# Kernel optimization log

Measured on AMD Instinct MI355X. Metric: run time of the kernel, lower is better.

## Reference

```python
import jax, jax.numpy as jnp
import numpy as np

NUM_CLASSES = 19
M = 5
TEMP = 100.0
MIN_RATIO = 0.75
IGNORE = 255
LOG2PI = float(np.log(2.0 * np.pi))


def l2_normalize(x, eps=1e-12):
    n = jnp.linalg.norm(x, axis=-1, keepdims=True)
    return x / jnp.maximum(n, eps)


def downscale_label_ratio(gt, scale):
    # gt: [B, H, W] int labels with IGNORE; avg-pool one-hot, keep majority class
    B, H, W = gt.shape
    out = jnp.where(gt == IGNORE, NUM_CLASSES, gt)
    oh = jax.nn.one_hot(out, NUM_CLASSES + 1, dtype=jnp.float32)  # [B,H,W,C+1]
    h, w = H // scale, W // scale
    pooled = oh.reshape(B, h, scale, w, scale, NUM_CLASSES + 1).mean(axis=(2, 4))
    ratio = pooled.max(axis=-1)          # [B,h,w] majority-class ratio
    idx = jnp.argmax(pooled, axis=-1)    # first max, like torch.max
    idx = jnp.where(idx == NUM_CLASSES, IGNORE, idx)
    idx = jnp.where(ratio < MIN_RATIO, IGNORE, idx)
    return idx


def gmm_log_prob(x, loc, scale):
    # Diagonal-Gaussian log-prob of x:[N,A] under K components loc/scale:[K,A] -> [N,K]
    inv_var = 1.0 / (scale * scale)
    maha = ((x * x) @ inv_var.T
            - 2.0 * (x @ (loc * inv_var).T)
            + jnp.sum(loc * loc * inv_var, axis=-1)[None, :])
    log_det = 2.0 * jnp.sum(jnp.log(scale), axis=-1)  # [K]
    A = x.shape[-1]
    return -0.5 * (A * LOG2PI + log_det[None, :] + maha)


def setup_inputs() -> dict:
    key = jax.random.key(0)
    ks = jax.random.split(key, 8)
    B, A, Hf, Wf = 4, 64, 256, 256
    Hm = Wm = 1024
    feat = jax.random.normal(ks[0], (B, A, Hf, Wf), jnp.float32)
    lab = jax.random.randint(ks[1], (B, Hm, Wm), 0, NUM_CLASSES)
    ign = jax.random.uniform(ks[2], (B, Hm, Wm)) < 0.05
    mask = jnp.where(ign, IGNORE, lab).astype(jnp.int32)
    mean = jax.random.normal(ks[3], (NUM_CLASSES, M, A), jnp.float32)
    covariance = 0.5 + jax.random.uniform(ks[4], (NUM_CLASSES, M, A), jnp.float32)
    target_memory = jax.random.normal(ks[5], (NUM_CLASSES, A, 100), jnp.float32)
    class_target = jax.random.uniform(ks[6], (NUM_CLASSES,), jnp.float32)
    class_sourse = 0.1 + jax.random.uniform(ks[7], (NUM_CLASSES,), jnp.float32)
    return {"feat": feat, "mask": mask, "mean": mean, "covariance": covariance,
            "target_memory": target_memory, "class_target": class_target,
            "class_sourse": class_sourse}


def reference(feat, mask, mean, covariance, target_memory, class_target, class_sourse):
    # ProtoGMM_loss: source=False, target_memory is not None, weak_target=False
    B, A, Hf, Wf = feat.shape
    scale = mask.shape[-1] // Wf
    m = downscale_label_ratio(mask, scale).reshape(-1)          # [N]
    f = feat.transpose(0, 2, 3, 1).reshape(-1, A)               # [N,A]
    f = l2_normalize(f)
    fd = jax.lax.stop_gradient(f)                               # feat.detach()
    loc = jax.lax.stop_gradient(mean).reshape(-1, A)            # [C*M,A]
    sc = jax.lax.stop_gradient(covariance).reshape(-1, A)

    log_prob = gmm_log_prob(fd, loc, sc)                        # [N,C*M]
    value = jax.nn.softmax(log_prob, axis=-1).reshape(-1, NUM_CLASSES, M)
    dist_ratio = jnp.nan_to_num(jax.lax.stop_gradient(class_target)
                                / jax.lax.stop_gradient(class_sourse))
    value = dist_ratio[None, :, None] * value                   # class-ratio scaling
    mean_target = l2_normalize(jax.lax.stop_gradient(target_memory).mean(axis=2))  # [C,A]
    sim = jax.nn.softmax(fd @ mean_target.T, axis=-1)           # [N,C]
    value = value * sim[:, :, None]
    labels = jnp.argmax(value.sum(-1), axis=-1)                 # pseudo-labels [N]

    logits = (f @ loc.T / TEMP).reshape(-1, NUM_CLASSES, M)     # [N,C,M]
    logits_max = logits.max(-1)                                 # [N,C]
    logls = jax.nn.log_softmax(logits_max, axis=-1)
    ce = -jnp.take_along_axis(logls, labels[:, None], axis=1)[:, 0]  # [N]
    valid = (m != IGNORE)
    loss = jnp.sum(jnp.where(valid, ce, 0.0)) / jnp.maximum(
        jnp.sum(valid).astype(jnp.float32), 1.0)
    return loss
```

## Files before the change

### kernel.cpp

```cpp
#include <hip/hip_runtime.h>
#include <hip/hip_bf16.h>
#include <math.h>

#define NCLS 19
#define MCOMP 5
#define AFEAT 64
#define IGNORE_L 255
#define LOG2PI 1.8378770664093453f

#define ROWS 160
#define WAM_B 0
#define WAL_B 40960
#define CST_B 61440
#define MT_B  62080
#define DR_B  64640
#define ACC_B 64768
#define VAL_B 64832

typedef __attribute__((ext_vector_type(8))) short bf16x8;
typedef __attribute__((ext_vector_type(4))) float f32x4;

__device__ inline float b2f(short s) {
    return __uint_as_float(((unsigned int)(unsigned short)s) << 16);
}
__device__ inline short f2b(float f) {
    __hip_bfloat16 h = __float2bfloat16(f);
    return *reinterpret_cast<short*>(&h);
}

__global__ void precompute_kernel(const float* __restrict__ mean,
                                  const float* __restrict__ cov,
                                  const float* __restrict__ tmem,
                                  const float* __restrict__ ct,
                                  const float* __restrict__ cs,
                                  char* __restrict__ wsb) {
    int blk = blockIdx.x;
    int a = threadIdx.x;
    short* wam = (short*)(wsb + WAM_B);
    short* wal = (short*)(wsb + WAL_B);
    float* cst = (float*)(wsb + CST_B);
    short* mtb = (short*)(wsb + MT_B);
    float* dr  = (float*)(wsb + DR_B);
    float* acc = (float*)(wsb + ACC_B);

    if (blk < ROWS) {
        int r = blk, c = r >> 3, m = r & 7;
        if (c < NCLS && m < MCOMP) {
            int k = c * MCOMP + m;
            float lo = mean[k * AFEAT + a];
            float cv = cov[k * AFEAT + a];
            float iv = 1.0f / (cv * cv);
            wam[r * 128 + a]      = f2b(-2.0f * lo * iv);
            wam[r * 128 + 64 + a] = f2b(iv);
            wal[r * 64 + a]       = f2b(lo);
            float s1 = lo * lo * iv;
            float s2 = logf(cv);
            for (int off = 32; off > 0; off >>= 1) {
                s1 += __shfl_xor(s1, off, 64);
                s2 += __shfl_xor(s2, off, 64);
            }
            if (a == 0) cst[r] = AFEAT * LOG2PI + 2.0f * s2 + s1;
        } else {
            wam[r * 128 + a] = 0; wam[r * 128 + 64 + a] = 0;
            wal[r * 64 + a] = 0;
            if (a == 0) cst[r] = 1e30f;
        }
    } else if (blk < ROWS + 20) {
        int c = blk - ROWS;
        if (c < NCLS) {
            const float* p = tmem + ((size_t)c * AFEAT + a) * 100;
            float s = 0.f;
            for (int j = 0; j < 100; ++j) s += p[j];
            s *= 0.01f;
            float n2 = s * s;
            for (int off = 32; off > 0; off >>= 1) n2 += __shfl_xor(n2, off, 64);
            float den = fmaxf(sqrtf(n2), 1e-12f);
            mtb[c * AFEAT + a] = f2b(s / den);
        } else {
            mtb[c * AFEAT + a] = 0;
        }
    } else {
        if (a < 20) {
            float r = 0.f;
            if (a < NCLS) {
                r = ct[a] / cs[a];
                if (isnan(r)) r = 0.f;
                else if (isinf(r)) r = (r > 0.f) ? 3.402823466e38f : -3.402823466e38f;
            }
            dr[a] = r;
        }
        if (a == 32) { acc[0] = 0.f; acc[1] = 0.f; }
    }
}

__global__ void valid_kernel(const int* __restrict__ mask,
                             unsigned long long* __restrict__ vwords) {
    int n = blockIdx.x * 256 + threadIdx.x;
    int b = n >> 16, rem = n & 65535, y = rem >> 8, x = rem & 255;
    const int* mp = mask + (((size_t)b << 10) + ((size_t)y << 2)) * 1024 + ((size_t)x << 2);
    int v[16];
#pragma unroll
    for (int r = 0; r < 4; ++r) {
        int4 q = *reinterpret_cast<const int4*>(mp + (size_t)r * 1024);
        v[r * 4 + 0] = q.x; v[r * 4 + 1] = q.y; v[r * 4 + 2] = q.z; v[r * 4 + 3] = q.w;
    }
    bool valid = false;
#pragma unroll
    for (int i = 0; i < 16; ++i) {
        int cnt = 0;
#pragma unroll
        for (int j = 0; j < 16; ++j) cnt += (v[j] == v[i]) ? 1 : 0;
        if (v[i] != IGNORE_L && cnt >= 12) valid = true;
    }
    unsigned long long bm = __ballot(valid);
    if ((threadIdx.x & 63) == 0) vwords[n >> 6] = bm;
}

__global__ __launch_bounds__(512, 2)
void protogmm_kernel(const float* __restrict__ feat,
                     const char* __restrict__ wsb,
                     const unsigned long long* __restrict__ vwords,
                     float* __restrict__ accg) {
    __shared__ short wamL[ROWS * 128];
    __shared__ short walL[ROWS * 64];
    __shared__ float cstL[ROWS];
    __shared__ short mtL[20 * 64];
    __shared__ float drL[20];

    int tid = threadIdx.x;
    {
        const uint4* s0 = (const uint4*)(wsb + WAM_B);
        for (int i = tid; i < 2560; i += 512) {
            int row = i >> 4, slot = i & 15;
            *(uint4*)((char*)wamL + row * 256 + ((slot ^ (row & 7)) << 4)) = s0[i];
        }
        const uint4* s1 = (const uint4*)(wsb + WAL_B);
        for (int i = tid; i < 1280; i += 512) {
            int row = i >> 3, slot = i & 7;
            *(uint4*)((char*)walL + row * 128 + ((slot ^ (row & 7)) << 4)) = s1[i];
        }
        const float* s2 = (const float*)(wsb + CST_B);
        for (int i = tid; i < ROWS; i += 512) cstL[i] = s2[i];
        const uint4* s3 = (const uint4*)(wsb + MT_B);
        for (int i = tid; i < 160; i += 512) ((uint4*)mtL)[i] = s3[i];
        const float* s4 = (const float*)(wsb + DR_B);
        if (tid < 20) drL[tid] = s4[tid];
    }
    __syncthreads();

    int lane = tid & 63, l15 = lane & 15, g = lane >> 4, rx = l15 & 7;
    int wv = blockIdx.x * 8 + (tid >> 6);
    int p = g >> 1;

    float cesum = 0.f, cntsum = 0.f;

#pragma unroll 1
    for (int it = 0; it < 4; ++it) {
        int tile = wv * 4 + it;
        int n0 = tile << 4;
        int b = n0 >> 16, y = (n0 >> 8) & 255, x0 = n0 & 255;

        bf16x8 F[4];
        {
            const float* fb = feat + (size_t)b * (AFEAT * 65536) + y * 256 + x0 + l15;
            float fa[8], fc[8];
            float n2 = 0.f;
#pragma unroll
            for (int j = 0; j < 8; ++j) {
                fa[j] = fb[(size_t)(8 * g + j) * 65536];
                fc[j] = fb[(size_t)(32 + 8 * g + j) * 65536];
            }
#pragma unroll
            for (int j = 0; j < 8; ++j) {
                n2 = fmaf(fa[j], fa[j], n2);
                n2 = fmaf(fc[j], fc[j], n2);
            }
            n2 += __shfl_xor(n2, 16, 64);
            n2 += __shfl_xor(n2, 32, 64);
            float inv = 1.0f / fmaxf(sqrtf(n2), 1e-12f);
#pragma unroll
            for (int j = 0; j < 8; ++j) {
                float u = fa[j] * inv, w2 = fc[j] * inv;
                F[0][j] = f2b(u);
                F[1][j] = f2b(w2);
                F[2][j] = f2b(u * u);
                F[3][j] = f2b(w2 * w2);
            }
        }

        float grun = -1e30f;
        float bestv = -1.0f, bestc = 0.f, bestl = 0.f, ls = 0.f;

#pragma unroll 1
        for (int t = 0; t < 10; ++t) {
            f32x4 acc = *(const f32x4*)(cstL + 16 * t + 4 * g);
#pragma unroll
            for (int kt = 0; kt < 4; ++kt) {
                bf16x8 wa = *(const bf16x8*)((char*)wamL + (16 * t + l15) * 256 +
                                             (((4 * kt + g) ^ rx) << 4));
                acc = __builtin_amdgcn_mfma_f32_16x16x32_bf16(wa, F[kt], acc, 0, 0, 0);
            }

            f32x4 a2 = {0.f, 0.f, 0.f, 0.f};
#pragma unroll
            for (int kt = 0; kt < 2; ++kt) {
                bf16x8 wl = *(const bf16x8*)((char*)walL + (16 * t + l15) * 128 +
                                             (((4 * kt + g) ^ rx) << 4));
                a2 = __builtin_amdgcn_mfma_f32_16x16x32_bf16(wl, F[kt], a2, 0, 0, 0);
            }
            float d0 = a2[0] * 0.01f, d1 = a2[1] * 0.01f;
            float d2 = a2[2] * 0.01f, d3 = a2[3] * 0.01f;
            if (g & 1) { d1 = -1e30f; d2 = -1e30f; d3 = -1e30f; }
            float lt = fmaxf(fmaxf(d0, d1), fmaxf(d2, d3));
            if (t == 9 && (g & 2)) lt = -1e30f;
            float lmx = fmaxf(lt, __shfl_xor(lt, 16, 64));
            ls += __expf(lmx);

            float mn = fminf(fminf(acc[0], acc[1]), fminf(acc[2], acc[3]));
            mn = fminf(mn, __shfl_xor(mn, 16, 64));
            mn = fminf(mn, __shfl_xor(mn, 32, 64));
            float gnew = fmaxf(grun, -0.5f * mn);
            float sold = __expf(grun - gnew);

            float e0 = __expf(fmaf(acc[0], -0.5f, -gnew));
            float e1 = __expf(fmaf(acc[1], -0.5f, -gnew));
            float e2 = __expf(fmaf(acc[2], -0.5f, -gnew));
            float e3 = __expf(fmaf(acc[3], -0.5f, -gnew));
            float st = (e0 + e1) + (e2 + e3);
            float Sc = st + __shfl_xor(st, 16, 64);

            const short* m0a = mtL + (2 * t) * 64 + 8 * g;
            const short* m1a = mtL + (2 * t + 1) * 64 + 8 * g;
            float p0 = 0.f, p1 = 0.f;
#pragma unroll
            for (int j = 0; j < 8; ++j) {
                float u = b2f(F[0][j]), w2 = b2f(F[1][j]);
                p0 = fmaf(u, b2f(m0a[j]), p0);
                p0 = fmaf(w2, b2f(m0a[32 + j]), p0);
                p1 = fmaf(u, b2f(m1a[j]), p1);
                p1 = fmaf(w2, b2f(m1a[32 + j]), p1);
            }
            p0 += __shfl_xor(p0, 16, 64); p0 += __shfl_xor(p0, 32, 64);
            p1 += __shfl_xor(p1, 16, 64); p1 += __shfl_xor(p1, 32, 64);
            float sd = p ? p1 : p0;

            float val = drL[2 * t + p] * __expf(sd) * Sc;
            bestv *= sold;
            if (val > bestv) { bestv = val; bestc = (float)(2 * t + p); bestl = lmx; }
            grun = gnew;
        }

        {
            float ov = __shfl_xor(bestv, 32, 64);
            float oc = __shfl_xor(bestc, 32, 64);
            float ol = __shfl_xor(bestl, 32, 64);
            bool take = (ov > bestv) || (ov == bestv && oc < bestc);
            bestv = take ? ov : bestv;
            bestl = take ? ol : bestl;
            bestc = take ? oc : bestc;
            ls += __shfl_xor(ls, 32, 64);
        }
        float ce = __logf(ls) - bestl;

        unsigned long long w = vwords[tile >> 2];
        float vb = (float)((w >> ((n0 & 63) + l15)) & 1ull);
        float own = (g == 0) ? 1.f : 0.f;
        cesum  = fmaf(own * vb, ce, cesum);
        cntsum += own * vb;
    }

#pragma unroll
    for (int off = 32; off > 0; off >>= 1) {
        cesum  += __shfl_xor(cesum, off, 64);
        cntsum += __shfl_xor(cntsum, off, 64);
    }
    if (lane == 0) {
        atomicAdd(&accg[0], cesum);
        atomicAdd(&accg[1], cntsum);
    }
}

__global__ void finalize_kernel(const float* __restrict__ acc, float* __restrict__ out) {
    out[0] = acc[0] / fmaxf(acc[1], 1.0f);
}

extern "C" void kernel_launch(void* const* d_in, const int* in_sizes, int n_in,
                              void* d_out, int out_size, void* d_ws, size_t ws_size,
                              hipStream_t stream) {
    const float* feat = (const float*)d_in[0];
    const int*   mask = (const int*)d_in[1];
    const float* mean = (const float*)d_in[2];
    const float* cov  = (const float*)d_in[3];
    const float* tmem = (const float*)d_in[4];
    const float* ct   = (const float*)d_in[5];
    const float* cs   = (const float*)d_in[6];
    float* out = (float*)d_out;
    char*  wsb = (char*)d_ws;

    precompute_kernel<<<ROWS + 20 + 1, 64, 0, stream>>>(mean, cov, tmem, ct, cs, wsb);
    valid_kernel<<<1024, 256, 0, stream>>>(mask, (unsigned long long*)(wsb + VAL_B));
    protogmm_kernel<<<512, 512, 0, stream>>>(feat, wsb,
                                             (const unsigned long long*)(wsb + VAL_B),
                                             (float*)(wsb + ACC_B));
    finalize_kernel<<<1, 1, 0, stream>>>((const float*)(wsb + ACC_B), out);
}
```

Before: 248.9 us.

## Process two pixel tiles per iteration and score classes in log domain

```diff
diff --git a/kernel.cpp b/kernel.cpp
--- a/kernel.cpp
+++ b/kernel.cpp
@@ -116,7 +116,7 @@
     if ((threadIdx.x & 63) == 0) vwords[n >> 6] = bm;
 }
 
-__global__ __launch_bounds__(512, 2)
+__global__ __launch_bounds__(512, 4)
 void protogmm_kernel(const float* __restrict__ feat,
                      const char* __restrict__ wsb,
                      const unsigned long long* __restrict__ vwords,
@@ -125,7 +125,7 @@
     __shared__ short walL[ROWS * 64];
     __shared__ float cstL[ROWS];
     __shared__ short mtL[20 * 64];
-    __shared__ float drL[20];
+    __shared__ float ldrL[20];
 
     int tid = threadIdx.x;
     {
@@ -144,7 +144,7 @@
         const uint4* s3 = (const uint4*)(wsb + MT_B);
         for (int i = tid; i < 160; i += 512) ((uint4*)mtL)[i] = s3[i];
         const float* s4 = (const float*)(wsb + DR_B);
-        if (tid < 20) drL[tid] = s4[tid];
+        if (tid < 20) ldrL[tid] = __logf(s4[tid]);
     }
     __syncthreads();
 
@@ -155,118 +155,164 @@
     float cesum = 0.f, cntsum = 0.f;
 
 #pragma unroll 1
-    for (int it = 0; it < 4; ++it) {
-        int tile = wv * 4 + it;
-        int n0 = tile << 4;
+    for (int it = 0; it < 2; ++it) {
+        int n0 = (wv * 2 + it) << 5;
         int b = n0 >> 16, y = (n0 >> 8) & 255, x0 = n0 & 255;
 
-        bf16x8 F[4];
+        bf16x8 FA[4], FB[4];
         {
             const float* fb = feat + (size_t)b * (AFEAT * 65536) + y * 256 + x0 + l15;
-            float fa[8], fc[8];
-            float n2 = 0.f;
+            float aa[8], ac[8], ba[8], bc[8];
+            float nA = 0.f, nB = 0.f;
 #pragma unroll
             for (int j = 0; j < 8; ++j) {
-                fa[j] = fb[(size_t)(8 * g + j) * 65536];
-                fc[j] = fb[(size_t)(32 + 8 * g + j) * 65536];
+                aa[j] = fb[(size_t)(8 * g + j) * 65536];
+                ac[j] = fb[(size_t)(32 + 8 * g + j) * 65536];
+                ba[j] = fb[(size_t)(8 * g + j) * 65536 + 16];
+                bc[j] = fb[(size_t)(32 + 8 * g + j) * 65536 + 16];
             }
 #pragma unroll
             for (int j = 0; j < 8; ++j) {
-                n2 = fmaf(fa[j], fa[j], n2);
-                n2 = fmaf(fc[j], fc[j], n2);
-            }
-            n2 += __shfl_xor(n2, 16, 64);
-            n2 += __shfl_xor(n2, 32, 64);
-            float inv = 1.0f / fmaxf(sqrtf(n2), 1e-12f);
+                nA = fmaf(aa[j], aa[j], nA); nA = fmaf(ac[j], ac[j], nA);
+                nB = fmaf(ba[j], ba[j], nB); nB = fmaf(bc[j], bc[j], nB);
+            }
+            nA += __shfl_xor(nA, 16, 64); nA += __shfl_xor(nA, 32, 64);
+            nB += __shfl_xor(nB, 16, 64); nB += __shfl_xor(nB, 32, 64);
+            float iA = 1.0f / fmaxf(sqrtf(nA), 1e-12f);
+            float iB = 1.0f / fmaxf(sqrtf(nB), 1e-12f);
 #pragma unroll
             for (int j = 0; j < 8; ++j) {
-                float u = fa[j] * inv, w2 = fc[j] * inv;
-                F[0][j] = f2b(u);
-                F[1][j] = f2b(w2);
-                F[2][j] = f2b(u * u);
-                F[3][j] = f2b(w2 * w2);
-            }
-        }
-
-        float grun = -1e30f;
-        float bestv = -1.0f, bestc = 0.f, bestl = 0.f, ls = 0.f;
-
-#pragma unroll 1
+                float u, w2;
+                u = aa[j] * iA; w2 = ac[j] * iA;
+                FA[0][j] = f2b(u); FA[1][j] = f2b(w2);
+                FA[2][j] = f2b(u * u); FA[3][j] = f2b(w2 * w2);
+                u = ba[j] * iB; w2 = bc[j] * iB;
+                FB[0][j] = f2b(u); FB[1][j] = f2b(w2);
+                FB[2][j] = f2b(u * u); FB[3][j] = f2b(w2 * w2);
+            }
+        }
+
+        float bWA = -3.4e38f, bcA = 0.f, blA = 0.f, lsA = 0.f;
+        float bWB = -3.4e38f, bcB = 0.f, blB = 0.f, lsB = 0.f;
+
+#pragma unroll 2
         for (int t = 0; t < 10; ++t) {
-            f32x4 acc = *(const f32x4*)(cstL + 16 * t + 4 * g);
+            f32x4 cini = *(const f32x4*)(cstL + 16 * t + 4 * g);
+            f32x4 aA = cini, aB = cini;
 #pragma unroll
             for (int kt = 0; kt < 4; ++kt) {
                 bf16x8 wa = *(const bf16x8*)((char*)wamL + (16 * t + l15) * 256 +
                                              (((4 * kt + g) ^ rx) << 4));
-                acc = __builtin_amdgcn_mfma_f32_16x16x32_bf16(wa, F[kt], acc, 0, 0, 0);
-            }
-
-            f32x4 a2 = {0.f, 0.f, 0.f, 0.f};
+                aA = __builtin_amdgcn_mfma_f32_16x16x32_bf16(wa, FA[kt], aA, 0, 0, 0);
+                aB = __builtin_amdgcn_mfma_f32_16x16x32_bf16(wa, FB[kt], aB, 0, 0, 0);
+            }
+            f32x4 qA = {0.f, 0.f, 0.f, 0.f}, qB = {0.f, 0.f, 0.f, 0.f};
 #pragma unroll
             for (int kt = 0; kt < 2; ++kt) {
                 bf16x8 wl = *(const bf16x8*)((char*)walL + (16 * t + l15) * 128 +
                                              (((4 * kt + g) ^ rx) << 4));
-                a2 = __builtin_amdgcn_mfma_f32_16x16x32_bf16(wl, F[kt], a2, 0, 0, 0);
-            }
-            float d0 = a2[0] * 0.01f, d1 = a2[1] * 0.01f;
-            float d2 = a2[2] * 0.01f, d3 = a2[3] * 0.01f;
-            if (g & 1) { d1 = -1e30f; d2 = -1e30f; d3 = -1e30f; }
-            float lt = fmaxf(fmaxf(d0, d1), fmaxf(d2, d3));
-            if (t == 9 && (g & 2)) lt = -1e30f;
-            float lmx = fmaxf(lt, __shfl_xor(lt, 16, 64));
-            ls += __expf(lmx);
-
-            float mn = fminf(fminf(acc[0], acc[1]), fminf(acc[2], acc[3]));
-            mn = fminf(mn, __shfl_xor(mn, 16, 64));
-            mn = fminf(mn, __shfl_xor(mn, 32, 64));
-            float gnew = fmaxf(grun, -0.5f * mn);
-            float sold = __expf(grun - gnew);
-
-            float e0 = __expf(fmaf(acc[0], -0.5f, -gnew));
-            float e1 = __expf(fmaf(acc[1], -0.5f, -gnew));
-            float e2 = __expf(fmaf(acc[2], -0.5f, -gnew));
-            float e3 = __expf(fmaf(acc[3], -0.5f, -gnew));
-            float st = (e0 + e1) + (e2 + e3);
-            float Sc = st + __shfl_xor(st, 16, 64);
-
-            const short* m0a = mtL + (2 * t) * 64 + 8 * g;
-            const short* m1a = mtL + (2 * t + 1) * 64 + 8 * g;
-            float p0 = 0.f, p1 = 0.f;
-#pragma unroll
-            for (int j = 0; j < 8; ++j) {
-                float u = b2f(F[0][j]), w2 = b2f(F[1][j]);
-                p0 = fmaf(u, b2f(m0a[j]), p0);
-                p0 = fmaf(w2, b2f(m0a[32 + j]), p0);
-                p1 = fmaf(u, b2f(m1a[j]), p1);
-                p1 = fmaf(w2, b2f(m1a[32 + j]), p1);
-            }
-            p0 += __shfl_xor(p0, 16, 64); p0 += __shfl_xor(p0, 32, 64);
-            p1 += __shfl_xor(p1, 16, 64); p1 += __shfl_xor(p1, 32, 64);
-            float sd = p ? p1 : p0;
-
-            float val = drL[2 * t + p] * __expf(sd) * Sc;
-            bestv *= sold;
-            if (val > bestv) { bestv = val; bestc = (float)(2 * t + p); bestl = lmx; }
-            grun = gnew;
+                qA = __builtin_amdgcn_mfma_f32_16x16x32_bf16(wl, FA[kt], qA, 0, 0, 0);
+                qB = __builtin_amdgcn_mfma_f32_16x16x32_bf16(wl, FB[kt], qB, 0, 0, 0);
+            }
+
+            bool mpad = (g & 1), cpad = (t == 9) && (g & 2);
+            float lmA, lmB;
+            {
+                float d0 = qA[0] * 0.01f, d1 = qA[1] * 0.01f;
+                float d2 = qA[2] * 0.01f, d3 = qA[3] * 0.01f;
+                if (mpad) { d1 = -1e30f; d2 = -1e30f; d3 = -1e30f; }
+                float lt = fmaxf(fmaxf(d0, d1), fmaxf(d2, d3));
+                if (cpad) lt = -1e30f;
+                lmA = fmaxf(lt, __shfl_xor(lt, 16, 64));
+                d0 = qB[0] * 0.01f; d1 = qB[1] * 0.01f;
+                d2 = qB[2] * 0.01f; d3 = qB[3] * 0.01f;
+                if (mpad) { d1 = -1e30f; d2 = -1e30f; d3 = -1e30f; }
+                lt = fmaxf(fmaxf(d0, d1), fmaxf(d2, d3));
+                if (cpad) lt = -1e30f;
+                lmB = fmaxf(lt, __shfl_xor(lt, 16, 64));
+            }
+            lsA += __expf(lmA);
+            lsB += __expf(lmB);
+
+            float lseA, lseB;
+            {
+                float mn = fminf(fminf(aA[0], aA[1]), fminf(aA[2], aA[3]));
+                mn = fminf(mn, __shfl_xor(mn, 16, 64));
+                float mx = -0.5f * mn;
+                float e0 = __expf(fmaf(aA[0], -0.5f, -mx));
+                float e1 = __expf(fmaf(aA[1], -0.5f, -mx));
+                float e2 = __expf(fmaf(aA[2], -0.5f, -mx));
+                float e3 = __expf(fmaf(aA[3], -0.5f, -mx));
+                float st = (e0 + e1) + (e2 + e3);
+                lseA = mx + __logf(st + __shfl_xor(st, 16, 64));
+                mn = fminf(fminf(aB[0], aB[1]), fminf(aB[2], aB[3]));
+                mn = fminf(mn, __shfl_xor(mn, 16, 64));
+                mx = -0.5f * mn;
+                e0 = __expf(fmaf(aB[0], -0.5f, -mx));
+                e1 = __expf(fmaf(aB[1], -0.5f, -mx));
+                e2 = __expf(fmaf(aB[2], -0.5f, -mx));
+                e3 = __expf(fmaf(aB[3], -0.5f, -mx));
+                st = (e0 + e1) + (e2 + e3);
+                lseB = mx + __logf(st + __shfl_xor(st, 16, 64));
+            }
+
+            float sdA, sdB;
+            {
+                const short* m0 = mtL + (2 * t) * 64 + 8 * g;
+                const short* m1 = mtL + (2 * t + 1) * 64 + 8 * g;
+                float p0A = 0.f, p1A = 0.f, p0B = 0.f, p1B = 0.f;
+#pragma unroll
+                for (int j = 0; j < 8; ++j) {
+                    float w0 = b2f(m0[j]), w1 = b2f(m0[32 + j]);
+                    float v0 = b2f(m1[j]), v1 = b2f(m1[32 + j]);
+                    float uA = b2f(FA[0][j]), cA = b2f(FA[1][j]);
+                    float uB = b2f(FB[0][j]), cB = b2f(FB[1][j]);
+                    p0A = fmaf(uA, w0, p0A); p0A = fmaf(cA, w1, p0A);
+                    p1A = fmaf(uA, v0, p1A); p1A = fmaf(cA, v1, p1A);
+                    p0B = fmaf(uB, w0, p0B); p0B = fmaf(cB, w1, p0B);
+                    p1B = fmaf(uB, v0, p1B); p1B = fmaf(cB, v1, p1B);
+                }
+                p0A += __shfl_xor(p0A, 16, 64); p0A += __shfl_xor(p0A, 32, 64);
+                p1A += __shfl_xor(p1A, 16, 64); p1A += __shfl_xor(p1A, 32, 64);
+                p0B += __shfl_xor(p0B, 16, 64); p0B += __shfl_xor(p0B, 32, 64);
+                p1B += __shfl_xor(p1B, 16, 64); p1B += __shfl_xor(p1B, 32, 64);
+                sdA = p ? p1A : p0A;
+                sdB = p ? p1B : p0B;
+            }
+
+            float ldr = ldrL[2 * t + p];
+            float WA = ldr + sdA + lseA;
+            float WB = ldr + sdB + lseB;
+            float cls = (float)(2 * t + p);
+            if (WA > bWA) { bWA = WA; bcA = cls; blA = lmA; }
+            if (WB > bWB) { bWB = WB; bcB = cls; blB = lmB; }
         }
 
         {
-            float ov = __shfl_xor(bestv, 32, 64);
-            float oc = __shfl_xor(bestc, 32, 64);
-            float ol = __shfl_xor(bestl, 32, 64);
-            bool take = (ov > bestv) || (ov == bestv && oc < bestc);
-            bestv = take ? ov : bestv;
-            bestl = take ? ol : bestl;
-            bestc = take ? oc : bestc;
-            ls += __shfl_xor(ls, 32, 64);
-        }
-        float ce = __logf(ls) - bestl;
-
-        unsigned long long w = vwords[tile >> 2];
-        float vb = (float)((w >> ((n0 & 63) + l15)) & 1ull);
-        float own = (g == 0) ? 1.f : 0.f;
-        cesum  = fmaf(own * vb, ce, cesum);
-        cntsum += own * vb;
+            float ov = __shfl_xor(bWA, 32, 64);
+            float oc = __shfl_xor(bcA, 32, 64);
+            float ol = __shfl_xor(blA, 32, 64);
+            bool take = (ov > bWA) || (ov == bWA && oc < bcA);
+            bWA = take ? ov : bWA; blA = take ? ol : blA; bcA = take ? oc : bcA;
+            lsA += __shfl_xor(lsA, 32, 64);
+            ov = __shfl_xor(bWB, 32, 64);
+            oc = __shfl_xor(bcB, 32, 64);
+            ol = __shfl_xor(blB, 32, 64);
+            take = (ov > bWB) || (ov == bWB && oc < bcB);
+            bWB = take ? ov : bWB; blB = take ? ol : blB; bcB = take ? oc : bcB;
+            lsB += __shfl_xor(lsB, 32, 64);
+        }
+        float ceA = __logf(lsA) - blA;
+        float ceB = __logf(lsB) - blB;
+
+        unsigned long long w = vwords[n0 >> 6];
+        float vbA = (float)((w >> ((n0 & 63) + l15)) & 1ull);
+        float vbB = (float)((w >> ((n0 & 63) + 16 + l15)) & 1ull);
+        if (g == 0) {
+            cesum = fmaf(vbA, ceA, cesum);
+            cesum = fmaf(vbB, ceB, cesum);
+            cntsum += vbA + vbB;
+        }
     }
 
 #pragma unroll
```

New measurement: 345.7 us. 1.39x slower.

## Fold target-similarity dot into MFMA, switch to log-space argmax, one tile per wave

Applied to the files above, without the earlier changes.

```diff
diff --git a/kernel.cpp b/kernel.cpp
--- a/kernel.cpp
+++ b/kernel.cpp
@@ -12,20 +12,21 @@
 #define WAM_B 0
 #define WAL_B 40960
 #define CST_B 61440
-#define MT_B  62080
-#define DR_B  64640
-#define ACC_B 64768
-#define VAL_B 64832
+#define DR_B  62080
+#define ACC_B 62208
+#define VAL_B 62272
 
 typedef __attribute__((ext_vector_type(8))) short bf16x8;
 typedef __attribute__((ext_vector_type(4))) float f32x4;
 
-__device__ inline float b2f(short s) {
-    return __uint_as_float(((unsigned int)(unsigned short)s) << 16);
-}
 __device__ inline short f2b(float f) {
     __hip_bfloat16 h = __float2bfloat16(f);
     return *reinterpret_cast<short*>(&h);
+}
+
+__device__ __host__ inline int wal_off(int r, int a) {
+    int tile = r >> 4, rr = r & 15, s = a >> 3, j = a & 7;
+    return ((tile * 8 + s) * 16 + rr) * 8 + j;
 }
 
 __global__ void precompute_kernel(const float* __restrict__ mean,
@@ -39,7 +40,6 @@
     short* wam = (short*)(wsb + WAM_B);
     short* wal = (short*)(wsb + WAL_B);
     float* cst = (float*)(wsb + CST_B);
-    short* mtb = (short*)(wsb + MT_B);
     float* dr  = (float*)(wsb + DR_B);
     float* acc = (float*)(wsb + ACC_B);
 
@@ -52,7 +52,7 @@
             float iv = 1.0f / (cv * cv);
             wam[r * 128 + a]      = f2b(-2.0f * lo * iv);
             wam[r * 128 + 64 + a] = f2b(iv);
-            wal[r * 64 + a]       = f2b(lo);
+            wal[wal_off(r, a)]    = f2b(lo);
             float s1 = lo * lo * iv;
             float s2 = logf(cv);
             for (int off = 32; off > 0; off >>= 1) {
@@ -62,11 +62,12 @@
             if (a == 0) cst[r] = AFEAT * LOG2PI + 2.0f * s2 + s1;
         } else {
             wam[r * 128 + a] = 0; wam[r * 128 + 64 + a] = 0;
-            wal[r * 64 + a] = 0;
+            if (!(m == 5 && c < NCLS)) wal[wal_off(r, a)] = 0;
             if (a == 0) cst[r] = 1e30f;
         }
     } else if (blk < ROWS + 20) {
         int c = blk - ROWS;
+        int r = ((c >> 1) << 4) + 8 * (c & 1) + 5;
         if (c < NCLS) {
             const float* p = tmem + ((size_t)c * AFEAT + a) * 100;
             float s = 0.f;
@@ -75,19 +76,19 @@
             float n2 = s * s;
             for (int off = 32; off > 0; off >>= 1) n2 += __shfl_xor(n2, off, 64);
             float den = fmaxf(sqrtf(n2), 1e-12f);
-            mtb[c * AFEAT + a] = f2b(s / den);
+            wal[wal_off(r, a)] = f2b(s / den);
         } else {
-            mtb[c * AFEAT + a] = 0;
+            wal[wal_off(r, a)] = 0;
         }
     } else {
         if (a < 20) {
-            float r = 0.f;
+            float rr = 0.f;
             if (a < NCLS) {
-                r = ct[a] / cs[a];
-                if (isnan(r)) r = 0.f;
-                else if (isinf(r)) r = (r > 0.f) ? 3.402823466e38f : -3.402823466e38f;
+                rr = ct[a] / cs[a];
+                if (isnan(rr)) rr = 0.f;
+                else if (isinf(rr)) rr = (rr > 0.f) ? 3.402823466e38f : -3.402823466e38f;
             }
-            dr[a] = r;
+            dr[a] = rr;
         }
         if (a == 32) { acc[0] = 0.f; acc[1] = 0.f; }
     }
@@ -116,16 +117,14 @@
     if ((threadIdx.x & 63) == 0) vwords[n >> 6] = bm;
 }
 
-__global__ __launch_bounds__(512, 2)
+__global__ __launch_bounds__(512, 6)
 void protogmm_kernel(const float* __restrict__ feat,
                      const char* __restrict__ wsb,
                      const unsigned long long* __restrict__ vwords,
                      float* __restrict__ accg) {
     __shared__ short wamL[ROWS * 128];
-    __shared__ short walL[ROWS * 64];
     __shared__ float cstL[ROWS];
-    __shared__ short mtL[20 * 64];
-    __shared__ float drL[20];
+    __shared__ float ldrL[20];
 
     int tid = threadIdx.x;
     {
@@ -134,140 +133,107 @@
             int row = i >> 4, slot = i & 15;
             *(uint4*)((char*)wamL + row * 256 + ((slot ^ (row & 7)) << 4)) = s0[i];
         }
-        const uint4* s1 = (const uint4*)(wsb + WAL_B);
-        for (int i = tid; i < 1280; i += 512) {
-            int row = i >> 3, slot = i & 7;
-            *(uint4*)((char*)walL + row * 128 + ((slot ^ (row & 7)) << 4)) = s1[i];
-        }
         const float* s2 = (const float*)(wsb + CST_B);
-        for (int i = tid; i < ROWS; i += 512) cstL[i] = s2[i];
-        const uint4* s3 = (const uint4*)(wsb + MT_B);
-        for (int i = tid; i < 160; i += 512) ((uint4*)mtL)[i] = s3[i];
+        if (tid < ROWS) cstL[tid] = s2[tid];
         const float* s4 = (const float*)(wsb + DR_B);
-        if (tid < 20) drL[tid] = s4[tid];
+        if (tid < 20) ldrL[tid] = __logf(s4[tid]);
     }
     __syncthreads();
 
     int lane = tid & 63, l15 = lane & 15, g = lane >> 4, rx = l15 & 7;
     int wv = blockIdx.x * 8 + (tid >> 6);
+    int n0 = wv << 4;
+    int b = n0 >> 16, y = (n0 >> 8) & 255, x0 = n0 & 255;
+    const char* walG = wsb + WAL_B;
+
+    bf16x8 F[4];
+    {
+        const float* fb = feat + (size_t)b * (AFEAT * 65536) + y * 256 + x0 + l15;
+        float fa[8], fc[8];
+        float n2 = 0.f;
+#pragma unroll
+        for (int j = 0; j < 8; ++j) {
+            fa[j] = fb[(size_t)(8 * g + j) * 65536];
+            fc[j] = fb[(size_t)(32 + 8 * g + j) * 65536];
+        }
+#pragma unroll
+        for (int j = 0; j < 8; ++j) {
+            n2 = fmaf(fa[j], fa[j], n2);
+            n2 = fmaf(fc[j], fc[j], n2);
+        }
+        n2 += __shfl_xor(n2, 16, 64);
+        n2 += __shfl_xor(n2, 32, 64);
+        float inv = 1.0f / fmaxf(sqrtf(n2), 1e-12f);
+#pragma unroll
+        for (int j = 0; j < 8; ++j) {
+            float u = fa[j] * inv, w2 = fc[j] * inv;
+            F[0][j] = f2b(u);
+            F[1][j] = f2b(w2);
+            F[2][j] = f2b(u * u);
+            F[3][j] = f2b(w2 * w2);
+        }
+    }
+
     int p = g >> 1;
-
-    float cesum = 0.f, cntsum = 0.f;
+    float ls = 0.f;
+    float bW = -3.4e38f, bc = 0.f, bl = 0.f;
 
 #pragma unroll 1
-    for (int it = 0; it < 4; ++it) {
-        int tile = wv * 4 + it;
-        int n0 = tile << 4;
-        int b = n0 >> 16, y = (n0 >> 8) & 255, x0 = n0 & 255;
-
-        bf16x8 F[4];
-        {
-            const float* fb = feat + (size_t)b * (AFEAT * 65536) + y * 256 + x0 + l15;
-            float fa[8], fc[8];
-            float n2 = 0.f;
-#pragma unroll
-            for (int j = 0; j < 8; ++j) {
-                fa[j] = fb[(size_t)(8 * g + j) * 65536];
-                fc[j] = fb[(size_t)(32 + 8 * g + j) * 65536];
-            }
-#pragma unroll
-            for (int j = 0; j < 8; ++j) {
-                n2 = fmaf(fa[j], fa[j], n2);
-                n2 = fmaf(fc[j], fc[j], n2);
-            }
-            n2 += __shfl_xor(n2, 16, 64);
-            n2 += __shfl_xor(n2, 32, 64);
-            float inv = 1.0f / fmaxf(sqrtf(n2), 1e-12f);
-#pragma unroll
-            for (int j = 0; j < 8; ++j) {
-                float u = fa[j] * inv, w2 = fc[j] * inv;
-                F[0][j] = f2b(u);
-                F[1][j] = f2b(w2);
-                F[2][j] = f2b(u * u);
-                F[3][j] = f2b(w2 * w2);
-            }
-        }
-
-        float grun = -1e30f;
-        float bestv = -1.0f, bestc = 0.f, bestl = 0.f, ls = 0.f;
-
-#pragma unroll 1
-        for (int t = 0; t < 10; ++t) {
-            f32x4 acc = *(const f32x4*)(cstL + 16 * t + 4 * g);
-#pragma unroll
-            for (int kt = 0; kt < 4; ++kt) {
-                bf16x8 wa = *(const bf16x8*)((char*)wamL + (16 * t + l15) * 256 +
-                                             (((4 * kt + g) ^ rx) << 4));
-                acc = __builtin_amdgcn_mfma_f32_16x16x32_bf16(wa, F[kt], acc, 0, 0, 0);
-            }
-
-            f32x4 a2 = {0.f, 0.f, 0.f, 0.f};
-#pragma unroll
-            for (int kt = 0; kt < 2; ++kt) {
-                bf16x8 wl = *(const bf16x8*)((char*)walL + (16 * t + l15) * 128 +
-                                             (((4 * kt + g) ^ rx) << 4));
-                a2 = __builtin_amdgcn_mfma_f32_16x16x32_bf16(wl, F[kt], a2, 0, 0, 0);
-            }
-            float d0 = a2[0] * 0.01f, d1 = a2[1] * 0.01f;
-            float d2 = a2[2] * 0.01f, d3 = a2[3] * 0.01f;
-            if (g & 1) { d1 = -1e30f; d2 = -1e30f; d3 = -1e30f; }
-            float lt = fmaxf(fmaxf(d0, d1), fmaxf(d2, d3));
-            if (t == 9 && (g & 2)) lt = -1e30f;
-            float lmx = fmaxf(lt, __shfl_xor(lt, 16, 64));
-            ls += __expf(lmx);
-
-            float mn = fminf(fminf(acc[0], acc[1]), fminf(acc[2], acc[3]));
-            mn = fminf(mn, __shfl_xor(mn, 16, 64));
-            mn = fminf(mn, __shfl_xor(mn, 32, 64));
-            float gnew = fmaxf(grun, -0.5f * mn);
-            float sold = __expf(grun - gnew);
-
-            float e0 = __expf(fmaf(acc[0], -0.5f, -gnew));
-            float e1 = __expf(fmaf(acc[1], -0.5f, -gnew));
-            float e2 = __expf(fmaf(acc[2], -0.5f, -gnew));
-            float e3 = __expf(fmaf(acc[3], -0.5f, -gnew));
-            float st = (e0 + e1) + (e2 + e3);
-            float Sc = st + __shfl_xor(st, 16, 64);
-
-            const short* m0a = mtL + (2 * t) * 64 + 8 * g;
-            const short* m1a = mtL + (2 * t + 1) * 64 + 8 * g;
-            float p0 = 0.f, p1 = 0.f;
-#pragma unroll
-            for (int j = 0; j < 8; ++j) {
-                float u = b2f(F[0][j]), w2 = b2f(F[1][j]);
-                p0 = fmaf(u, b2f(m0a[j]), p0);
-                p0 = fmaf(w2, b2f(m0a[32 + j]), p0);
-                p1 = fmaf(u, b2f(m1a[j]), p1);
-                p1 = fmaf(w2, b2f(m1a[32 + j]), p1);
-            }
-            p0 += __shfl_xor(p0, 16, 64); p0 += __shfl_xor(p0, 32, 64);
-            p1 += __shfl_xor(p1, 16, 64); p1 += __shfl_xor(p1, 32, 64);
-            float sd = p ? p1 : p0;
-
-            float val = drL[2 * t + p] * __expf(sd) * Sc;
-            bestv *= sold;
-            if (val > bestv) { bestv = val; bestc = (float)(2 * t + p); bestl = lmx; }
-            grun = gnew;
-        }
-
-        {
-            float ov = __shfl_xor(bestv, 32, 64);
-            float oc = __shfl_xor(bestc, 32, 64);
-            float ol = __shfl_xor(bestl, 32, 64);
-            bool take = (ov > bestv) || (ov == bestv && oc < bestc);
-            bestv = take ? ov : bestv;
-            bestl = take ? ol : bestl;
-            bestc = take ? oc : bestc;
-            ls += __shfl_xor(ls, 32, 64);
-        }
-        float ce = __logf(ls) - bestl;
-
-        unsigned long long w = vwords[tile >> 2];
-        float vb = (float)((w >> ((n0 & 63) + l15)) & 1ull);
-        float own = (g == 0) ? 1.f : 0.f;
-        cesum  = fmaf(own * vb, ce, cesum);
-        cntsum += own * vb;
-    }
+    for (int t = 0; t < 10; ++t) {
+        f32x4 acc = *(const f32x4*)(cstL + 16 * t + 4 * g);
+#pragma unroll
+        for (int kt = 0; kt < 4; ++kt) {
+            bf16x8 wa = *(const bf16x8*)((char*)wamL + (16 * t + l15) * 256 +
+                                         (((4 * kt + g) ^ rx) << 4));
+            acc = __builtin_amdgcn_mfma_f32_16x16x32_bf16(wa, F[kt], acc, 0, 0, 0);
+        }
+
+        f32x4 q = {0.f, 0.f, 0.f, 0.f};
+#pragma unroll
+        for (int kt = 0; kt < 2; ++kt) {
+            bf16x8 wl = *(const bf16x8*)(walG +
+                        (((t * 8 + 4 * kt + g) * 16 + l15) << 4));
+            q = __builtin_amdgcn_mfma_f32_16x16x32_bf16(wl, F[kt], q, 0, 0, 0);
+        }
+        float sd = q[1];
+
+        float d0 = q[0] * 0.01f, d1 = q[1] * 0.01f;
+        float d2 = q[2] * 0.01f, d3 = q[3] * 0.01f;
+        if (g & 1) { d1 = -1e30f; d2 = -1e30f; d3 = -1e30f; }
+        float lt = fmaxf(fmaxf(d0, d1), fmaxf(d2, d3));
+        if (t == 9 && (g & 2)) lt = -1e30f;
+        float lmx = fmaxf(lt, __shfl_xor(lt, 16, 64));
+        ls += __expf(lmx);
+
+        float mn = fminf(fminf(acc[0], acc[1]), fminf(acc[2], acc[3]));
+        mn = fminf(mn, __shfl_xor(mn, 16, 64));
+        float mx = -0.5f * mn;
+        float e0 = __expf(fmaf(acc[0], -0.5f, -mx));
+        float e1 = __expf(fmaf(acc[1], -0.5f, -mx));
+        float e2 = __expf(fmaf(acc[2], -0.5f, -mx));
+        float e3 = __expf(fmaf(acc[3], -0.5f, -mx));
+        float st = (e0 + e1) + (e2 + e3);
+        float lse = mx + __logf(st + __shfl_xor(st, 16, 64));
+
+        float W = ldrL[2 * t + p] + sd + lse;
+        if (W > bW) { bW = W; bc = (float)(2 * t + p); bl = lmx; }
+    }
+
+    {
+        float ov = __shfl_xor(bW, 32, 64);
+        float oc = __shfl_xor(bc, 32, 64);
+        float ol = __shfl_xor(bl, 32, 64);
+        bool take = (ov > bW) || (ov == bW && oc < bc);
+        bW = take ? ov : bW; bl = take ? ol : bl; bc = take ? oc : bc;
+        ls += __shfl_xor(ls, 32, 64);
+    }
+    float ce = __logf(ls) - bl;
+
+    unsigned long long w = vwords[wv >> 2];
+    float vb = (float)((w >> (((wv & 3) << 4) + l15)) & 1ull);
+    float own = (g == 1) ? 1.f : 0.f;
+    float cesum  = own * vb * ce;
+    float cntsum = own * vb;
 
 #pragma unroll
     for (int off = 32; off > 0; off >>= 1) {
@@ -299,8 +265,8 @@
 
     precompute_kernel<<<ROWS + 20 + 1, 64, 0, stream>>>(mean, cov, tmem, ct, cs, wsb);
     valid_kernel<<<1024, 256, 0, stream>>>(mask, (unsigned long long*)(wsb + VAL_B));
-    protogmm_kernel<<<512, 512, 0, stream>>>(feat, wsb,
-                                             (const unsigned long long*)(wsb + VAL_B),
-                                             (float*)(wsb + ACC_B));
+    protogmm_kernel<<<2048, 512, 0, stream>>>(feat, wsb,
+                                              (const unsigned long long*)(wsb + VAL_B),
+                                              (float*)(wsb + ACC_B));
     finalize_kernel<<<1, 1, 0, stream>>>((const float*)(wsb + ACC_B), out);
 }
```

Result: slower. 535.4 us (+115.1%).
